# Performance work log

Measured on AMD Instinct MI355X. Metric: run time of the kernel, lower is better.

## Reference

```python
import jax, jax.numpy as jnp
import numpy as np

B, T, D, VQ, L2, HID = 8, 2048, 768, 64, 12, 1024
K = 2 ** L2          # 4096 codebook entries
N_MID = 4            # condition_layer=6 -> 1 input + 4 middle + 1 output Linear, 5 BatchNorms
EPS_N = 1e-6
EPS_BN = 1e-5


def setup_inputs() -> dict:
    key = jax.random.key(0)
    ks = jax.random.split(key, 10)
    g = lambda i, shape, sc: jax.random.normal(ks[i], shape, jnp.float32) * sc
    return {
        "h_in": jax.random.normal(ks[0], (B, D, T), jnp.float32),
        "attn_mask": jax.random.randint(ks[1], (B, T), 0, 2, jnp.int32),
        "proj_w": g(2, (VQ, D), 0.02), "proj_b": jnp.zeros((VQ,), jnp.float32),
        "inv_w": g(3, (D, VQ), 0.02), "inv_b": jnp.zeros((D,), jnp.float32),
        "mlp_w_in": g(4, (HID, L2), 0.1), "mlp_b_in": jnp.zeros((HID,), jnp.float32),
        "mlp_w_mid": g(5, (N_MID, HID, HID), 0.03), "mlp_b_mid": jnp.zeros((N_MID, HID), jnp.float32),
        "mlp_w_out": g(6, (VQ, HID), 0.03), "mlp_b_out": jnp.zeros((VQ,), jnp.float32),
        "bn_gamma": jnp.ones((N_MID + 1, HID), jnp.float32),
        "bn_beta": jnp.zeros((N_MID + 1, HID), jnp.float32),
    }


def _bn(x, gamma, beta):
    # BatchNorm1d, training mode: batch mean / biased var over codebook rows
    m = x.mean(axis=0)
    v = x.var(axis=0)
    return (x - m) * jax.lax.rsqrt(v + EPS_BN) * gamma + beta


def _l2norm(x):
    return x / (jnp.linalg.norm(x, axis=-1, keepdims=True) + EPS_N)


def reference(h_in, attn_mask, proj_w, proj_b, inv_w, inv_b,
              mlp_w_in, mlp_b_in, mlp_w_mid, mlp_b_mid, mlp_w_out, mlp_b_out,
              bn_gamma, bn_beta):
    # --- codebook: binary vectors -> condition MLP (Linear+BN+ReLU x5, Linear) ---
    ints = jnp.arange(K)
    bits = ((ints[:, None] & (1 << jnp.arange(L2 - 1, -1, -1))) > 0).astype(jnp.float32)  # [K, L2]
    x = jax.nn.relu(_bn(bits @ mlp_w_in.T + mlp_b_in, bn_gamma[0], bn_beta[0]))
    for i in range(N_MID):
        x = jax.nn.relu(_bn(x @ mlp_w_mid[i].T + mlp_b_mid[i], bn_gamma[i + 1], bn_beta[i + 1]))
    embed = x @ mlp_w_out.T + mlp_b_out          # [K, VQ]
    embed = _l2norm(embed)                        # sphere=True

    # --- project hidden states: h_in [B,D,T] -> [B,T,VQ] ---
    h = jnp.einsum('bdt,vd->btv', h_in, proj_w) + proj_b
    h = _l2norm(h)

    # --- pairwise squared distances to codebook, argmax of -d (== softmax argmax) ---
    hf = h.reshape(-1, VQ)                                       # [B*T, VQ]
    d = (hf ** 2).sum(-1, keepdims=True) + (embed ** 2).sum(-1) - 2.0 * (hf @ embed.T)  # [B*T, K]
    code = jnp.argmax(-d, axis=-1)                               # [B*T]

    # --- masked gather/scatter quantization (eval path: hard codes) ---
    mask = (attn_mask == 1)                                      # [B, T]
    h_vq = embed[code].reshape(B, T, VQ) * mask[..., None].astype(h.dtype)
    quantized = jnp.einsum('btv,dv->btd', h_vq, inv_w) + inv_b   # proj_inv -> [B, T, D]
    vq_code = jnp.where(mask, code.reshape(B, T), 0)
    return quantized, vq_code
```

## Files before the change

### kernel.cpp

```cpp
#include <hip/hip_runtime.h>
#include <stddef.h>

#define BB   8
#define TT_  2048
#define DD   768
#define VQ_  64
#define L2C  12
#define HID_ 1024
#define KK   4096
#define NMID 4
#define NT   (BB*TT_)

typedef _Float16 h8v __attribute__((ext_vector_type(8)));
typedef float    f4v __attribute__((ext_vector_type(4)));

#define GL16(g, l) __builtin_amdgcn_global_load_lds( \
    (const __attribute__((address_space(1))) void*)(g), \
    (__attribute__((address_space(3))) void*)(l), 16, 0, 0)

__global__ __launch_bounds__(256) void k_mlp_in(const float* __restrict__ w_in,
                                                const float* __restrict__ b_in,
                                                float* __restrict__ X) {
    __shared__ float ws_[256 * 12];
    __shared__ float bs_[256];
    int tid = threadIdx.x;
    int h0  = blockIdx.x * 256;
    for (int i = tid; i < 256 * 12; i += 256) ws_[i] = w_in[h0 * 12 + i];
    bs_[tid] = b_in[h0 + tid];
    __syncthreads();
    float w[12];
#pragma unroll
    for (int l = 0; l < 12; l++) w[l] = ws_[tid * 12 + l];
    float bias = bs_[tid];
    int k0 = blockIdx.y * 16;
    for (int kk = 0; kk < 16; kk++) {
        int k = k0 + kk;
        float acc = bias;
#pragma unroll
        for (int l = 0; l < 12; l++)
            if ((k >> (11 - l)) & 1) acc += w[l];
        X[(size_t)k * HID_ + h0 + tid] = acc;
    }
}

__global__ __launch_bounds__(256) void k_bn_stats1(const float* __restrict__ Y,
                                                   float* __restrict__ part) {
    int b = blockIdx.x;
    int c = blockIdx.y * 256 + threadIdx.x;
    const float* src = Y + ((size_t)b << 6) * HID_ + c;
    float s = 0.f, q = 0.f;
    for (int r = 0; r < 64; r++) {
        float v = src[(size_t)r << 10];
        s += v; q += v * v;
    }
    part[((size_t)b << 10) + c] = s;
    part[65536 + ((size_t)b << 10) + c] = q;
}

__global__ __launch_bounds__(256) void k_bn_stats2(const float* __restrict__ part,
                                                   float* __restrict__ mv) {
    int c = blockIdx.x * 256 + threadIdx.x;
    float s = 0.f, q = 0.f;
    for (int b = 0; b < 64; b++) {
        s += part[((size_t)b << 10) + c];
        q += part[65536 + ((size_t)b << 10) + c];
    }
    float m = s * (1.f / KK);
    float v = q * (1.f / KK) - m * m;
    mv[c] = m; mv[HID_ + c] = v;
}

__global__ __launch_bounds__(256) void k_bn_apply_split(const float* __restrict__ Y,
                                                        const float* __restrict__ mv,
                                                        const float* __restrict__ gamma,
                                                        const float* __restrict__ beta,
                                                        _Float16* __restrict__ Xhi,
                                                        _Float16* __restrict__ Xlo) {
    int i = blockIdx.x * 256 + threadIdx.x;
    int c = (i << 2) & (HID_ - 1);
    float4 x = ((const float4*)Y)[i];
    float4 m = *(const float4*)(mv + c);
    float4 v = *(const float4*)(mv + HID_ + c);
    float4 g = *(const float4*)(gamma + c);
    float4 b = *(const float4*)(beta + c);
    float o[4];
    o[0] = fmaxf(0.f, (x.x - m.x) * (1.f / sqrtf(v.x + 1e-5f)) * g.x + b.x);
    o[1] = fmaxf(0.f, (x.y - m.y) * (1.f / sqrtf(v.y + 1e-5f)) * g.y + b.y);
    o[2] = fmaxf(0.f, (x.z - m.z) * (1.f / sqrtf(v.z + 1e-5f)) * g.z + b.z);
    o[3] = fmaxf(0.f, (x.w - m.w) * (1.f / sqrtf(v.w + 1e-5f)) * g.w + b.w);
    union { _Float16 h[4]; uint2 u; } uh, ul;
#pragma unroll
    for (int j = 0; j < 4; j++) {
        _Float16 h = (_Float16)o[j];
        uh.h[j] = h;
        ul.h[j] = (_Float16)(o[j] - (float)h);
    }
    *(uint2*)(Xhi + ((size_t)i << 2)) = uh.u;
    *(uint2*)(Xlo + ((size_t)i << 2)) = ul.u;
}

__global__ __launch_bounds__(256) void k_gemm_mfma3(const _Float16* __restrict__ Ahi,
                                                    const _Float16* __restrict__ Alo,
                                                    const _Float16* __restrict__ Whi,
                                                    const _Float16* __restrict__ Wlo,
                                                    const float* __restrict__ bias,
                                                    float* __restrict__ C) {
    __shared__ __attribute__((aligned(128))) char lds[4 * 32768];
    const int tid = threadIdx.x;
    const int wg = blockIdx.x;
    const int m0 = (wg & 31) << 7;
    const int n0 = (wg >> 5) << 7;
    const int wave = tid >> 6, lane = tid & 63;
    const int l15 = lane & 15, quad = lane >> 4;
    const int wm = (wave >> 1) << 6;
    const int wn = (wave & 1) << 6;

    const int rowA = (wave << 5) + (lane >> 2);
    const int colb = (((lane & 3) ^ (rowA & 3)) << 4);
    const char* gA_h = (const char*)Ahi + ((size_t)(m0 + rowA) << 11) + colb;
    const char* gA_l = (const char*)Alo + ((size_t)(m0 + rowA) << 11) + colb;
    const char* gW_h = (const char*)Whi + ((size_t)(n0 + rowA) << 11) + colb;
    const char* gW_l = (const char*)Wlo + ((size_t)(n0 + rowA) << 11) + colb;
    const int dA = wave << 11;

    const int rsw = l15 & 3;
    int offA[4], offW[4];
#pragma unroll
    for (int i = 0; i < 4; i++) offA[i] = ((wm + (i << 4) + l15) << 6) + ((quad ^ rsw) << 4);
#pragma unroll
    for (int j = 0; j < 4; j++) offW[j] = ((wn + (j << 4) + l15) << 6) + ((quad ^ rsw) << 4);

    f4v acc[4][4];
#pragma unroll
    for (int i = 0; i < 4; i++)
#pragma unroll
        for (int j = 0; j < 4; j++) acc[i][j] = (f4v){0.f, 0.f, 0.f, 0.f};

#define STG(bufi, tt) do { \
        char* b_ = lds + ((bufi) << 15); int o_ = (tt) << 6; \
        GL16(gA_h + o_,         b_ + dA); \
        GL16(gA_h + 32768 + o_, b_ + dA + 1024); \
        GL16(gA_l + o_,         b_ + 8192 + dA); \
        GL16(gA_l + 32768 + o_, b_ + 8192 + dA + 1024); \
        GL16(gW_h + o_,         b_ + 16384 + dA); \
        GL16(gW_h + 32768 + o_, b_ + 16384 + dA + 1024); \
        GL16(gW_l + o_,         b_ + 24576 + dA); \
        GL16(gW_l + 32768 + o_, b_ + 24576 + dA + 1024); \
    } while (0)

    STG(0, 0); STG(1, 1); STG(2, 2);
    for (int t = 0; t < 32; ++t) {
        if (t <= 29)      asm volatile("s_waitcnt vmcnt(16)" ::: "memory");
        else if (t == 30) asm volatile("s_waitcnt vmcnt(8)"  ::: "memory");
        else              asm volatile("s_waitcnt vmcnt(0)"  ::: "memory");
        __builtin_amdgcn_s_barrier();
        asm volatile("" ::: "memory");
        if (t + 3 < 32) STG((t + 3) & 3, t + 3);
        const char* b = lds + ((size_t)(t & 3) << 15);
        h8v ah[4], al[4], bh[4], bl[4];
#pragma unroll
        for (int i = 0; i < 4; i++) {
            ah[i] = *(const h8v*)(b + offA[i]);
            al[i] = *(const h8v*)(b + 8192 + offA[i]);
        }
#pragma unroll
        for (int j = 0; j < 4; j++) {
            bh[j] = *(const h8v*)(b + 16384 + offW[j]);
            bl[j] = *(const h8v*)(b + 24576 + offW[j]);
        }
        __builtin_amdgcn_s_setprio(1);
#pragma unroll
        for (int j = 0; j < 4; j++)
#pragma unroll
            for (int i = 0; i < 4; i++)
                acc[i][j] = __builtin_amdgcn_mfma_f32_16x16x32_f16(ah[i], bh[j], acc[i][j], 0, 0, 0);
#pragma unroll
        for (int j = 0; j < 4; j++)
#pragma unroll
            for (int i = 0; i < 4; i++)
                acc[i][j] = __builtin_amdgcn_mfma_f32_16x16x32_f16(ah[i], bl[j], acc[i][j], 0, 0, 0);
#pragma unroll
        for (int j = 0; j < 4; j++)
#pragma unroll
            for (int i = 0; i < 4; i++)
                acc[i][j] = __builtin_amdgcn_mfma_f32_16x16x32_f16(al[i], bh[j], acc[i][j], 0, 0, 0);
        __builtin_amdgcn_s_setprio(0);
        asm volatile("" ::: "memory");
    }
#undef STG

#pragma unroll
    for (int j = 0; j < 4; j++) {
        int col = n0 + wn + (j << 4) + l15;
        float bv = bias[col];
#pragma unroll
        for (int i = 0; i < 4; i++) {
            int row = m0 + wm + (i << 4) + (quad << 2);
#pragma unroll
            for (int r = 0; r < 4; r++)
                C[(size_t)(row + r) * HID_ + col] = acc[i][j][r] + bv;
        }
    }
}

__global__ __launch_bounds__(256) void k_gemm_mfma2(const _Float16* __restrict__ Ahi,
                                                    const _Float16* __restrict__ Alo,
                                                    const _Float16* __restrict__ Whi,
                                                    const _Float16* __restrict__ Wlo,
                                                    const float* __restrict__ bias,
                                                    float* __restrict__ C,
                                                    int M, int N, int Kd) {
    __shared__ __attribute__((aligned(128))) char lds[2][24576];
    const int tid = threadIdx.x;
    int wg = blockIdx.x;
    const int nwg = gridDim.x;
    wg = (wg & 7) * (nwg >> 3) + (wg >> 3);
    const int nx = M >> 7;
    const int m0 = (wg % nx) << 7;
    const int n0 = (wg / nx) << 6;
    const int wave = tid >> 6, lane = tid & 63;
    const int l15 = lane & 15, quad = lane >> 4;
    const int wm = (wave >> 1) << 6;
    const int wn = (wave & 1) << 5;

    const int pA0 = ((wave << 1) | 0) * 1024 + lane * 16;
    const int pA1 = ((wave << 1) | 1) * 1024 + lane * 16;
    const int pW  = wave * 1024 + lane * 16;
    const int qA0 = pA0 ^ (((pA0 >> 7) & 3) << 4);
    const int qA1 = pA1 ^ (((pA1 >> 7) & 3) << 4);
    const int qW  = pW  ^ (((pW  >> 7) & 3) << 4);
    const size_t krow = (size_t)Kd * 2;
    const char* gAh0 = (const char*)Ahi + (size_t)(m0 + (qA0 >> 6)) * krow + (qA0 & 63);
    const char* gAh1 = (const char*)Ahi + (size_t)(m0 + (qA1 >> 6)) * krow + (qA1 & 63);
    const char* gAl0 = (const char*)Alo + (size_t)(m0 + (qA0 >> 6)) * krow + (qA0 & 63);
    const char* gAl1 = (const char*)Alo + (size_t)(m0 + (qA1 >> 6)) * krow + (qA1 & 63);
    const char* gWh  = (const char*)Whi + (size_t)(n0 + (qW >> 6)) * krow + (qW & 63);
    const char* gWl  = (const char*)Wlo + (size_t)(n0 + (qW >> 6)) * krow + (qW & 63);
    const int dA0 = (wave << 1) * 1024;
    const int dA1 = dA0 + 1024;
    const int dW  = wave * 1024;

    int offA[4], offW[2];
#pragma unroll
    for (int i = 0; i < 4; i++) {
        int r = wm + (i << 4) + l15;
        offA[i] = r * 64 + ((quad ^ ((r >> 1) & 3)) << 4);
    }
#pragma unroll
    for (int j = 0; j < 2; j++) {
        int r = wn + (j << 4) + l15;
        offW[j] = r * 64 + ((quad ^ ((r >> 1) & 3)) << 4);
    }

    f4v acc[4][2];
#pragma unroll
    for (int i = 0; i < 4; i++)
#pragma unroll
        for (int j = 0; j < 2; j++) acc[i][j] = (f4v){0.f, 0.f, 0.f, 0.f};

#define STAGE(bufi, tt) do { \
        char* b_ = lds[bufi]; size_t o_ = (size_t)(tt) << 6; \
        GL16(gAh0 + o_, b_ + dA0); \
        GL16(gAh1 + o_, b_ + dA1); \
        GL16(gAl0 + o_, b_ + 8192 + dA0); \
        GL16(gAl1 + o_, b_ + 8192 + dA1); \
        GL16(gWh  + o_, b_ + 16384 + dW); \
        GL16(gWl  + o_, b_ + 20480 + dW); \
    } while (0)

    STAGE(0, 0);
    const int nt = Kd >> 5;
    for (int t = 0; t < nt; ++t) {
        const int cur = t & 1;
        if (t + 1 < nt) {
            STAGE(cur ^ 1, t + 1);
            asm volatile("s_waitcnt vmcnt(6)" ::: "memory");
        } else {
            asm volatile("s_waitcnt vmcnt(0)" ::: "memory");
        }
        __builtin_amdgcn_s_barrier();
        asm volatile("" ::: "memory");
        const char* b = lds[cur];
        h8v ah[4], al[4], bh[2], bl[2];
#pragma unroll
        for (int i = 0; i < 4; i++) {
            ah[i] = *(const h8v*)(b + offA[i]);
            al[i] = *(const h8v*)(b + 8192 + offA[i]);
        }
#pragma unroll
        for (int j = 0; j < 2; j++) {
            bh[j] = *(const h8v*)(b + 16384 + offW[j]);
            bl[j] = *(const h8v*)(b + 20480 + offW[j]);
        }
        __builtin_amdgcn_s_setprio(1);
#pragma unroll
        for (int i = 0; i < 4; i++)
#pragma unroll
            for (int j = 0; j < 2; j++)
                acc[i][j] = __builtin_amdgcn_mfma_f32_16x16x32_f16(ah[i], bh[j], acc[i][j], 0, 0, 0);
#pragma unroll
        for (int i = 0; i < 4; i++)
#pragma unroll
            for (int j = 0; j < 2; j++)
                acc[i][j] = __builtin_amdgcn_mfma_f32_16x16x32_f16(ah[i], bl[j], acc[i][j], 0, 0, 0);
#pragma unroll
        for (int i = 0; i < 4; i++)
#pragma unroll
            for (int j = 0; j < 2; j++)
                acc[i][j] = __builtin_amdgcn_mfma_f32_16x16x32_f16(al[i], bh[j], acc[i][j], 0, 0, 0);
        __builtin_amdgcn_s_setprio(0);
        asm volatile("" ::: "memory");
        __builtin_amdgcn_s_barrier();
    }
#undef STAGE

#pragma unroll
    for (int j = 0; j < 2; j++) {
        int col = n0 + wn + (j << 4) + l15;
        float bv = bias[col];
#pragma unroll
        for (int i = 0; i < 4; i++) {
            int row = m0 + wm + (i << 4) + (quad << 2);
#pragma unroll
            for (int r = 0; r < 4; r++)
                C[(size_t)(row + r) * N + col] = acc[i][j][r] + bv;
        }
    }
}

__global__ __launch_bounds__(256) void k_l2norm(float* __restrict__ E,
                                                float* __restrict__ eqh,
                                                _Float16* __restrict__ Ehi,
                                                _Float16* __restrict__ Elo) {
    int tid = threadIdx.x;
    int row = blockIdx.x * 4 + (tid >> 6);
    int v = tid & 63;
    size_t off = ((size_t)row << 6) + v;
    float x = E[off];
    float ss = x * x;
#pragma unroll
    for (int o = 32; o; o >>= 1) ss += __shfl_xor(ss, o, 64);
    float inv = 1.f / (sqrtf(ss) + 1e-6f);
    float xn = x * inv;
    E[off] = xn;
    _Float16 hh = (_Float16)xn;
    Ehi[off] = hh;
    Elo[off] = (_Float16)(xn - (float)hh);
    if (v == 0) eqh[row] = -0.5f * (ss * inv * inv);
}

__global__ __launch_bounds__(256) void k_wsplit_all(const float* __restrict__ w_mid,
                                                    const float* __restrict__ w_out,
                                                    const float* __restrict__ proj_w,
                                                    _Float16* __restrict__ Wmh,
                                                    _Float16* __restrict__ Wml,
                                                    _Float16* __restrict__ Woh,
                                                    _Float16* __restrict__ Wol,
                                                    _Float16* __restrict__ pwhi,
                                                    _Float16* __restrict__ pwlo) {
    int i = blockIdx.x * 256 + threadIdx.x;
    const float4* src; _Float16 *dh, *dl; int off;
    if (i < 1048576)            { src = (const float4*)w_mid;  dh = Wmh;  dl = Wml;  off = i; }
    else if (i < 1048576+16384) { src = (const float4*)w_out;  dh = Woh;  dl = Wol;  off = i - 1048576; }
    else                        { src = (const float4*)proj_w; dh = pwhi; dl = pwlo; off = i - 1048576 - 16384; }
    float4 w = src[off];
    float wf[4] = {w.x, w.y, w.z, w.w};
    union { _Float16 h[4]; uint2 u; } uh, ul;
#pragma unroll
    for (int j = 0; j < 4; j++) {
        _Float16 h = (_Float16)wf[j];
        uh.h[j] = h;
        ul.h[j] = (_Float16)(wf[j] - (float)h);
    }
    *(uint2*)(dh + ((size_t)off << 2)) = uh.u;
    *(uint2*)(dl + ((size_t)off << 2)) = ul.u;
}

__global__ __launch_bounds__(256) void k_cvt_inv(const float* __restrict__ iw,
                                                 _Float16* __restrict__ iwh) {
    int i = blockIdx.x * 256 + threadIdx.x;
    float4 w = ((const float4*)iw)[i];
    union { _Float16 h[4]; uint2 u; } uh;
    uh.h[0] = (_Float16)w.x; uh.h[1] = (_Float16)w.y;
    uh.h[2] = (_Float16)w.z; uh.h[3] = (_Float16)w.w;
    *(uint2*)(iwh + ((size_t)i << 2)) = uh.u;
}

__global__ __launch_bounds__(256) void k_proj_mfma(const float* __restrict__ h_in,
                                                   const _Float16* __restrict__ pwhi,
                                                   const _Float16* __restrict__ pwlo,
                                                   float* __restrict__ Hpart) {
    __shared__ float shA[128 * 33];
    const int tid = threadIdx.x;
    const int t0 = blockIdx.x * 128;
    const int ks = blockIdx.y;
    const int b = t0 >> 11;
    const int tloc0 = t0 & (TT_ - 1);
    const int wave = tid >> 6, lane = tid & 63;
    const int l15 = lane & 15, quad = lane >> 4;

    const int dl = tid >> 3;
    const int tg = (tid & 7) << 4;

    f4v acc[2][4];
#pragma unroll
    for (int i = 0; i < 2; i++)
#pragma unroll
        for (int j = 0; j < 4; j++) acc[i][j] = (f4v){0.f, 0.f, 0.f, 0.f};

    for (int kk = 0; kk < 6; kk++) {
        int dd0 = ks * 192 + kk * 32;
        const float* src = h_in + ((size_t)(b * DD + dd0 + dl) << 11) + tloc0 + tg;
        float4 g0 = *(const float4*)(src);
        float4 g1 = *(const float4*)(src + 4);
        float4 g2 = *(const float4*)(src + 8);
        float4 g3 = *(const float4*)(src + 12);
        __syncthreads();
        float gv[16] = {g0.x, g0.y, g0.z, g0.w, g1.x, g1.y, g1.z, g1.w,
                        g2.x, g2.y, g2.z, g2.w, g3.x, g3.y, g3.z, g3.w};
#pragma unroll
        for (int i = 0; i < 16; i++) shA[(tg + i) * 33 + dl] = gv[i];
        __syncthreads();

        h8v ah[2], al[2];
#pragma unroll
        for (int mt = 0; mt < 2; mt++) {
            const float* ap = &shA[((wave << 5) + (mt << 4) + l15) * 33 + (quad << 3)];
            float4 a0 = *(const float4*)(ap);
            float4 a1 = *(const float4*)(ap + 4);
            float av[8] = {a0.x, a0.y, a0.z, a0.w, a1.x, a1.y, a1.z, a1.w};
#pragma unroll
            for (int j = 0; j < 8; j++) {
                _Float16 h = (_Float16)av[j];
                ah[mt][j] = h;
                al[mt][j] = (_Float16)(av[j] - (float)h);
            }
        }
        h8v bh[4], bl[4];
#pragma unroll
        for (int nt = 0; nt < 4; nt++) {
            size_t wb = (size_t)((nt << 4) + l15) * DD + dd0 + (quad << 3);
            bh[nt] = *(const h8v*)(pwhi + wb);
            bl[nt] = *(const h8v*)(pwlo + wb);
        }
#pragma unroll
        for (int nt = 0; nt < 4; nt++)
#pragma unroll
            for (int mt = 0; mt < 2; mt++)
                acc[mt][nt] = __builtin_amdgcn_mfma_f32_16x16x32_f16(ah[mt], bh[nt], acc[mt][nt], 0, 0, 0);
#pragma unroll
        for (int nt = 0; nt < 4; nt++)
#pragma unroll
            for (int mt = 0; mt < 2; mt++)
                acc[mt][nt] = __builtin_amdgcn_mfma_f32_16x16x32_f16(ah[mt], bl[nt], acc[mt][nt], 0, 0, 0);
#pragma unroll
        for (int nt = 0; nt < 4; nt++)
#pragma unroll
            for (int mt = 0; mt < 2; mt++)
                acc[mt][nt] = __builtin_amdgcn_mfma_f32_16x16x32_f16(al[mt], bh[nt], acc[mt][nt], 0, 0, 0);
    }
    float* dst = Hpart + ((size_t)ks << 20);
#pragma unroll
    for (int mt = 0; mt < 2; mt++) {
#pragma unroll
        for (int r = 0; r < 4; r++) {
            int t = t0 + (wave << 5) + (mt << 4) + (quad << 2) + r;
#pragma unroll
            for (int nt = 0; nt < 4; nt++)
                dst[((size_t)t << 6) + (nt << 4) + l15] = acc[mt][nt][r];
        }
    }
}

__global__ __launch_bounds__(256) void k_hnorm(const float* __restrict__ Hpart,
                                               const float* __restrict__ pb,
                                               _Float16* __restrict__ Hhi,
                                               _Float16* __restrict__ Hlo) {
    __shared__ float ssp[4][64];
    int tid = threadIdx.x;
    int tt = tid & 63, vg = tid >> 6;
    int t = blockIdx.x * 64 + tt;
    size_t base = ((size_t)t << 6) + (vg << 4);
    float o[16];
#pragma unroll
    for (int u = 0; u < 4; u++) {
        float4 p0 = *(const float4*)(Hpart + (0u << 20) + base + (u << 2));
        float4 p1 = *(const float4*)(Hpart + (1u << 20) + base + (u << 2));
        float4 p2 = *(const float4*)(Hpart + (2u << 20) + base + (u << 2));
        float4 p3 = *(const float4*)(Hpart + (3u << 20) + base + (u << 2));
        o[u * 4 + 0] = p0.x + p1.x + p2.x + p3.x;
        o[u * 4 + 1] = p0.y + p1.y + p2.y + p3.y;
        o[u * 4 + 2] = p0.z + p1.z + p2.z + p3.z;
        o[u * 4 + 3] = p0.w + p1.w + p2.w + p3.w;
    }
    float sp = 0.f;
#pragma unroll
    for (int j = 0; j < 16; j++) {
        o[j] += pb[(vg << 4) + j];
        sp = fmaf(o[j], o[j], sp);
    }
    ssp[vg][tt] = sp;
    __syncthreads();
    float ss = ssp[0][tt] + ssp[1][tt] + ssp[2][tt] + ssp[3][tt];
    float inv = 1.f / (sqrtf(ss) + 1e-6f);
    union { _Float16 h[8]; uint4 u; } uh0, uh1, ul0, ul1;
#pragma unroll
    for (int j = 0; j < 16; j++) {
        float xn = o[j] * inv;
        _Float16 hh = (_Float16)xn;
        _Float16 ll = (_Float16)(xn - (float)hh);
        if (j < 8) { uh0.h[j] = hh; ul0.h[j] = ll; }
        else       { uh1.h[j - 8] = hh; ul1.h[j - 8] = ll; }
    }
    *(uint4*)(Hhi + base)     = uh0.u;
    *(uint4*)(Hhi + base + 8) = uh1.u;
    *(uint4*)(Hlo + base)     = ul0.u;
    *(uint4*)(Hlo + base + 8) = ul1.u;
}

__global__ __launch_bounds__(256, 4) void k_argmax_mfma(const _Float16* __restrict__ Hhi,
                                                        const _Float16* __restrict__ Hlo,
                                                        const _Float16* __restrict__ Ehi,
                                                        const _Float16* __restrict__ Elo,
                                                        const float* __restrict__ eqh,
                                                        float* __restrict__ ps,
                                                        int* __restrict__ pi) {
    __shared__ __attribute__((aligned(128))) char elds[4 * 4096 + 1024];
    int tid = threadIdx.x;
    int wave = tid >> 6, lane = tid & 63;
    int l15 = lane & 15, quad = lane >> 4;
    int t0 = blockIdx.x * 256 + wave * 64;
    int kh = blockIdx.y;
    const int kbase = kh << 8;

    h8v hh0[4], hh1[4], hl0[4], hl1[4];
#pragma unroll
    for (int s = 0; s < 4; s++) {
        size_t hb = (size_t)(t0 + (s << 4) + l15) * 64 + (quad << 3);
        hh0[s] = *(const h8v*)(Hhi + hb);
        hh1[s] = *(const h8v*)(Hhi + hb + 32);
        hl0[s] = *(const h8v*)(Hlo + hb);
        hl1[s] = *(const h8v*)(Hlo + hb + 32);
    }
    float best[4] = {-1e30f, -1e30f, -1e30f, -1e30f};
    int   idx[4]  = {0, 0, 0, 0};

    const int p    = ((wave & 1) << 10) + lane * 16;
    const int srow = p >> 7;
    const int scol = (p & 127) ^ ((srow & 7) << 4);
    const char* gsrc0 = (const char*)((wave < 2) ? Ehi : Elo)
                      + (((size_t)kbase + srow) << 7) + scol;
    const int dwave = wave << 10;
#define ASTG(tt) GL16(gsrc0 + ((size_t)(tt) << 11), elds + (((tt) & 3) << 12) + dwave)

    const int rswz = (l15 & 7) << 4;
    const int o_e0 = l15 * 128 + ((quad << 4) ^ rswz);
    const int o_e1 = l15 * 128 + ((64 + (quad << 4)) ^ rswz);

    if (wave == 0) GL16((const char*)eqh + ((size_t)kbase << 2), elds + 16384);
    ASTG(0); ASTG(1); ASTG(2);

    for (int t = 0; t < 16; ++t) {
        if (t <= 13)      asm volatile("s_waitcnt vmcnt(2)" ::: "memory");
        else if (t == 14) asm volatile("s_waitcnt vmcnt(1)" ::: "memory");
        else              asm volatile("s_waitcnt vmcnt(0)" ::: "memory");
        __builtin_amdgcn_s_barrier();
        asm volatile("" ::: "memory");
        if (t + 3 < 16) ASTG(t + 3);
        const char* b = elds + ((size_t)(t & 3) << 12);
        h8v ce0 = *(const h8v*)(b + o_e0);
        h8v ce1 = *(const h8v*)(b + o_e1);
        h8v cl0 = *(const h8v*)(b + 2048 + o_e0);
        h8v cl1 = *(const h8v*)(b + 2048 + o_e1);
        float4 cq = *(const float4*)(elds + 16384 + (t << 6) + (quad << 4));
        int k0 = kbase + (t << 4);

        f4v acc[4];
#pragma unroll
        for (int s = 0; s < 4; s++) acc[s] = (f4v){0.f, 0.f, 0.f, 0.f};
        __builtin_amdgcn_s_setprio(1);
#pragma unroll
        for (int s = 0; s < 4; s++) acc[s] = __builtin_amdgcn_mfma_f32_16x16x32_f16(ce0, hh0[s], acc[s], 0, 0, 0);
#pragma unroll
        for (int s = 0; s < 4; s++) acc[s] = __builtin_amdgcn_mfma_f32_16x16x32_f16(ce1, hh1[s], acc[s], 0, 0, 0);
#pragma unroll
        for (int s = 0; s < 4; s++) acc[s] = __builtin_amdgcn_mfma_f32_16x16x32_f16(cl0, hh0[s], acc[s], 0, 0, 0);
#pragma unroll
        for (int s = 0; s < 4; s++) acc[s] = __builtin_amdgcn_mfma_f32_16x16x32_f16(cl1, hh1[s], acc[s], 0, 0, 0);
#pragma unroll
        for (int s = 0; s < 4; s++) acc[s] = __builtin_amdgcn_mfma_f32_16x16x32_f16(ce0, hl0[s], acc[s], 0, 0, 0);
#pragma unroll
        for (int s = 0; s < 4; s++) acc[s] = __builtin_amdgcn_mfma_f32_16x16x32_f16(ce1, hl1[s], acc[s], 0, 0, 0);
        __builtin_amdgcn_s_setprio(0);
        float qv[4] = {cq.x, cq.y, cq.z, cq.w};
#pragma unroll
        for (int r = 0; r < 4; r++) {
            int k = k0 + (quad << 2) + r;
#pragma unroll
            for (int s = 0; s < 4; s++) {
                float sc = acc[s][r] + qv[r];
                if (sc > best[s]) { best[s] = sc; idx[s] = k; }
            }
        }
        asm volatile("" ::: "memory");
    }
#undef ASTG

#pragma unroll
    for (int m = 16; m <= 32; m <<= 1) {
#pragma unroll
        for (int s = 0; s < 4; s++) {
            float ob = __shfl_xor(best[s], m, 64);
            int   oi = __shfl_xor(idx[s], m, 64);
            if (ob > best[s] || (ob == best[s] && oi < idx[s])) { best[s] = ob; idx[s] = oi; }
        }
    }
    if (quad == 0) {
#pragma unroll
        for (int s = 0; s < 4; s++) {
            int t = t0 + (s << 4) + l15;
            ps[(size_t)t * 16 + kh] = best[s];
            pi[(size_t)t * 16 + kh] = idx[s];
        }
    }
}

__global__ __launch_bounds__(256) void k_merge(const float* __restrict__ ps,
                                               const int* __restrict__ pi,
                                               const int* __restrict__ mask,
                                               const _Float16* __restrict__ Ehi,
                                               _Float16* __restrict__ G16,
                                               float* __restrict__ outc) {
    __shared__ int codes[256];
    __shared__ int ms[256];
    int tid = threadIdx.x;
    int base = blockIdx.x << 8;
    int t = base + tid;
    float best = ps[(size_t)t * 16];
    int bi = pi[(size_t)t * 16];
#pragma unroll
    for (int s = 1; s < 16; s++) {
        float v = ps[(size_t)t * 16 + s];
        if (v > best) { best = v; bi = pi[(size_t)t * 16 + s]; }
    }
    int m = mask[t];
    codes[tid] = bi;
    ms[tid] = m;
    outc[t] = m ? (float)bi : 0.0f;
    __syncthreads();
    for (int i = tid; i < 256 * 8; i += 256) {
        int r = i >> 3, u = i & 7;
        uint4 e = ms[r] ? ((const uint4*)(Ehi + ((size_t)codes[r] << 6)))[u]
                        : make_uint4(0u, 0u, 0u, 0u);
        ((uint4*)(G16 + ((size_t)(base + r) << 6)))[u] = e;
    }
}

__global__ __launch_bounds__(256) void k_gemm_out(const _Float16* __restrict__ G16,
                                                  const _Float16* __restrict__ iwh,
                                                  const float* __restrict__ bias,
                                                  float* __restrict__ C) {
    const int tid = threadIdx.x;
    const int t0 = blockIdx.x * 128, n0 = blockIdx.y * 64;
    const int wave = tid >> 6, lane = tid & 63;
    const int l15 = lane & 15, quad = lane >> 4;

    f4v acc[2][4];
#pragma unroll
    for (int i = 0; i < 2; i++)
#pragma unroll
        for (int j = 0; j < 4; j++) acc[i][j] = (f4v){0.f, 0.f, 0.f, 0.f};

#pragma unroll
    for (int ks = 0; ks < 2; ks++) {
        int kk = (ks << 5) + (quad << 3);
        h8v a[2], b[4];
#pragma unroll
        for (int mt = 0; mt < 2; mt++)
            a[mt] = *(const h8v*)(G16 + (size_t)(t0 + (wave << 5) + (mt << 4) + l15) * 64 + kk);
#pragma unroll
        for (int nt = 0; nt < 4; nt++)
            b[nt] = *(const h8v*)(iwh + (size_t)(n0 + (nt << 4) + l15) * 64 + kk);
#pragma unroll
        for (int mt = 0; mt < 2; mt++)
#pragma unroll
            for (int nt = 0; nt < 4; nt++)
                acc[mt][nt] = __builtin_amdgcn_mfma_f32_16x16x32_f16(a[mt], b[nt], acc[mt][nt], 0, 0, 0);
    }
#pragma unroll
    for (int nt = 0; nt < 4; nt++) {
        int col = n0 + (nt << 4) + l15;
        float bv = bias[col];
#pragma unroll
        for (int mt = 0; mt < 2; mt++) {
            int row = t0 + (wave << 5) + (mt << 4) + (quad << 2);
#pragma unroll
            for (int r = 0; r < 4; r++)
                C[(size_t)(row + r) * DD + col] = acc[mt][nt][r] + bv;
        }
    }
}

extern "C" void kernel_launch(void* const* d_in, const int* in_sizes, int n_in,
                              void* d_out, int out_size, void* d_ws, size_t ws_size,
                              hipStream_t stream) {
    const float* h_in   = (const float*)d_in[0];
    const int*   amask  = (const int*)d_in[1];
    const float* proj_w = (const float*)d_in[2];
    const float* proj_b = (const float*)d_in[3];
    const float* inv_w  = (const float*)d_in[4];
    const float* inv_b  = (const float*)d_in[5];
    const float* w_in   = (const float*)d_in[6];
    const float* b_in   = (const float*)d_in[7];
    const float* w_mid  = (const float*)d_in[8];
    const float* b_mid  = (const float*)d_in[9];
    const float* w_out  = (const float*)d_in[10];
    const float* b_out  = (const float*)d_in[11];
    const float* gamma  = (const float*)d_in[12];
    const float* beta   = (const float*)d_in[13];

    float*     Y    = (float*)d_ws;
    _Float16*  Xhi  = (_Float16*)(Y + (size_t)KK * HID_);
    _Float16*  Xlo  = Xhi + (size_t)KK * HID_;
    float*     mv   = (float*)(Xlo + (size_t)KK * HID_);
    float*     Emb  = mv + 2 * HID_;
    float*     eqh  = Emb + (size_t)KK * VQ_;
    float*     spart= eqh + KK;
    _Float16*  pwhi = (_Float16*)(spart + 2 * 65536);
    _Float16*  pwlo = pwhi + (size_t)VQ_ * DD;
    float*    Hpart = Y;
    _Float16* H16hi = Xhi;
    _Float16* H16lo = H16hi + (size_t)NT * VQ_;
    _Float16* E16hi = H16lo + (size_t)NT * VQ_;
    _Float16* E16lo = E16hi + (size_t)KK * VQ_;
    float*    ps    = (float*)(E16lo + (size_t)KK * VQ_);
    int*      pidx  = (int*)(ps + (size_t)NT * 16);
    _Float16* G16   = (_Float16*)(pidx + (size_t)NT * 16);
    _Float16* iwh   = G16 + (size_t)NT * VQ_;

    float* out_q = (float*)d_out;
    float* out_c = out_q + (size_t)NT * DD;

    _Float16* Wmh = (_Float16*)d_out;
    _Float16* Wml = Wmh + (size_t)NMID * HID_ * HID_;
    _Float16* Woh = Wml + (size_t)NMID * HID_ * HID_;
    _Float16* Wol = Woh + (size_t)VQ_ * HID_;

    k_wsplit_all<<<4208, 256, 0, stream>>>(w_mid, w_out, proj_w,
                                           Wmh, Wml, Woh, Wol, pwhi, pwlo);

    k_mlp_in<<<dim3(HID_ / 256, KK / 16), 256, 0, stream>>>(w_in, b_in, Y);
    k_bn_stats1<<<dim3(64, 4), 256, 0, stream>>>(Y, spart);
    k_bn_stats2<<<4, 256, 0, stream>>>(spart, mv);
    k_bn_apply_split<<<KK * HID_ / 1024, 256, 0, stream>>>(Y, mv, gamma, beta, Xhi, Xlo);
    for (int i = 0; i < NMID; i++) {
        k_gemm_mfma3<<<(KK / 128) * (HID_ / 128), 256, 0, stream>>>(
            Xhi, Xlo, Wmh + (size_t)i * HID_ * HID_, Wml + (size_t)i * HID_ * HID_,
            b_mid + (size_t)i * HID_, Y);
        k_bn_stats1<<<dim3(64, 4), 256, 0, stream>>>(Y, spart);
        k_bn_stats2<<<4, 256, 0, stream>>>(spart, mv);
        k_bn_apply_split<<<KK * HID_ / 1024, 256, 0, stream>>>(Y, mv,
            gamma + (size_t)(i + 1) * HID_, beta + (size_t)(i + 1) * HID_, Xhi, Xlo);
    }
    k_gemm_mfma2<<<(KK / 128) * (VQ_ / 64), 256, 0, stream>>>(
        Xhi, Xlo, Woh, Wol, b_out, Emb, KK, VQ_, HID_);
    k_l2norm<<<KK / 4, 256, 0, stream>>>(Emb, eqh, E16hi, E16lo);

    k_cvt_inv<<<VQ_ * DD / 1024, 256, 0, stream>>>(inv_w, iwh);
    k_proj_mfma<<<dim3(NT / 128, 4), 256, 0, stream>>>(h_in, pwhi, pwlo, Hpart);
    k_hnorm<<<NT / 64, 256, 0, stream>>>(Hpart, proj_b, H16hi, H16lo);
    k_argmax_mfma<<<dim3(NT / 256, 16), 256, 0, stream>>>(
        H16hi, H16lo, E16hi, E16lo, eqh, ps, pidx);
    k_merge<<<NT / 256, 256, 0, stream>>>(ps, pidx, amask, E16hi, G16, out_c);
    k_gemm_out<<<dim3(NT / 128, DD / 64), 256, 0, stream>>>(G16, iwh, inv_b, out_q);
}
```

Measured before the change: 454.2 us.

## Rebalance GEMM pipelines: double-buffer mfma3, triple-buffer mfma2 with 64-wide K tiles

The 128x128 split-fp16 GEMM drops from a 4-stage LDS ring to a 2-stage double buffer with an extra barrier, cutting its LDS footprint from 128 KB to 64 KB. The 128x64 generic GEMM goes the other way: it now stages 64-wide K tiles with an 8-way XOR swizzle into a 3-deep ring, issuing loads two tiles ahead and removing the trailing barrier. The aim is to hide load latency better in mfma2 and raise occupancy or reduce LDS pressure in mfma3. The trade-off is less prefetch depth in mfma3 and 144 KB of LDS in mfma2, which limits it to one block per CU.

```diff
diff --git a/kernel.cpp b/kernel.cpp
--- a/kernel.cpp
+++ b/kernel.cpp
@@ -105,7 +105,7 @@
                                                     const _Float16* __restrict__ Wlo,
                                                     const float* __restrict__ bias,
                                                     float* __restrict__ C) {
-    __shared__ __attribute__((aligned(128))) char lds[4 * 32768];
+    __shared__ __attribute__((aligned(128))) char lds[2 * 32768];
     const int tid = threadIdx.x;
     const int wg = blockIdx.x;
     const int m0 = (wg & 31) << 7;
@@ -148,15 +148,17 @@
         GL16(gW_l + 32768 + o_, b_ + 24576 + dA + 1024); \
     } while (0)
 
-    STG(0, 0); STG(1, 1); STG(2, 2);
+    STG(0, 0);
     for (int t = 0; t < 32; ++t) {
-        if (t <= 29)      asm volatile("s_waitcnt vmcnt(16)" ::: "memory");
-        else if (t == 30) asm volatile("s_waitcnt vmcnt(8)"  ::: "memory");
-        else              asm volatile("s_waitcnt vmcnt(0)"  ::: "memory");
+        if (t + 1 < 32) {
+            STG((t + 1) & 1, t + 1);
+            asm volatile("s_waitcnt vmcnt(8)" ::: "memory");
+        } else {
+            asm volatile("s_waitcnt vmcnt(0)" ::: "memory");
+        }
         __builtin_amdgcn_s_barrier();
         asm volatile("" ::: "memory");
-        if (t + 3 < 32) STG((t + 3) & 3, t + 3);
-        const char* b = lds + ((size_t)(t & 3) << 15);
+        const char* b = lds + ((size_t)(t & 1) << 15);
         h8v ah[4], al[4], bh[4], bl[4];
 #pragma unroll
         for (int i = 0; i < 4; i++) {
@@ -186,6 +188,7 @@
                 acc[i][j] = __builtin_amdgcn_mfma_f32_16x16x32_f16(al[i], bh[j], acc[i][j], 0, 0, 0);
         __builtin_amdgcn_s_setprio(0);
         asm volatile("" ::: "memory");
+        __builtin_amdgcn_s_barrier();
     }
 #undef STG
 
@@ -210,7 +213,7 @@
                                                     const float* __restrict__ bias,
                                                     float* __restrict__ C,
                                                     int M, int N, int Kd) {
-    __shared__ __attribute__((aligned(128))) char lds[2][24576];
+    __shared__ __attribute__((aligned(128))) char lds[3 * 49152];
     const int tid = threadIdx.x;
     int wg = blockIdx.x;
     const int nwg = gridDim.x;
@@ -223,33 +226,30 @@
     const int wm = (wave >> 1) << 6;
     const int wn = (wave & 1) << 5;
 
-    const int pA0 = ((wave << 1) | 0) * 1024 + lane * 16;
-    const int pA1 = ((wave << 1) | 1) * 1024 + lane * 16;
-    const int pW  = wave * 1024 + lane * 16;
-    const int qA0 = pA0 ^ (((pA0 >> 7) & 3) << 4);
-    const int qA1 = pA1 ^ (((pA1 >> 7) & 3) << 4);
-    const int qW  = pW  ^ (((pW  >> 7) & 3) << 4);
     const size_t krow = (size_t)Kd * 2;
-    const char* gAh0 = (const char*)Ahi + (size_t)(m0 + (qA0 >> 6)) * krow + (qA0 & 63);
-    const char* gAh1 = (const char*)Ahi + (size_t)(m0 + (qA1 >> 6)) * krow + (qA1 & 63);
-    const char* gAl0 = (const char*)Alo + (size_t)(m0 + (qA0 >> 6)) * krow + (qA0 & 63);
-    const char* gAl1 = (const char*)Alo + (size_t)(m0 + (qA1 >> 6)) * krow + (qA1 & 63);
-    const char* gWh  = (const char*)Whi + (size_t)(n0 + (qW >> 6)) * krow + (qW & 63);
-    const char* gWl  = (const char*)Wlo + (size_t)(n0 + (qW >> 6)) * krow + (qW & 63);
-    const int dA0 = (wave << 1) * 1024;
-    const int dA1 = dA0 + 1024;
-    const int dW  = wave * 1024;
-
-    int offA[4], offW[2];
+    const int colb2 = (((lane & 7) ^ (lane >> 3)) << 4);
+    const char* gA_h = (const char*)Ahi + (size_t)(m0 + (wave << 5) + (lane >> 3)) * krow + colb2;
+    const char* gA_l = (const char*)Alo + (size_t)(m0 + (wave << 5) + (lane >> 3)) * krow + colb2;
+    const char* gW_h = (const char*)Whi + (size_t)(n0 + (wave << 4) + (lane >> 3)) * krow + colb2;
+    const char* gW_l = (const char*)Wlo + (size_t)(n0 + (wave << 4) + (lane >> 3)) * krow + colb2;
+    const int dAh = wave << 12;
+    const int dWh = wave << 11;
+    const size_t g8 = 8 * krow;
+
+    int offA[4][2], offW[2][2];
 #pragma unroll
     for (int i = 0; i < 4; i++) {
         int r = wm + (i << 4) + l15;
-        offA[i] = r * 64 + ((quad ^ ((r >> 1) & 3)) << 4);
+        int sw = (r & 7) << 4;
+        offA[i][0] = (r << 7) + (((quad << 4)) ^ sw);
+        offA[i][1] = (r << 7) + ((64 | (quad << 4)) ^ sw);
     }
 #pragma unroll
     for (int j = 0; j < 2; j++) {
         int r = wn + (j << 4) + l15;
-        offW[j] = r * 64 + ((quad ^ ((r >> 1) & 3)) << 4);
+        int sw = (r & 7) << 4;
+        offW[j][0] = (r << 7) + (((quad << 4)) ^ sw);
+        offW[j][1] = (r << 7) + ((64 | (quad << 4)) ^ sw);
     }
 
     f4v acc[4][2];
@@ -258,61 +258,65 @@
 #pragma unroll
         for (int j = 0; j < 2; j++) acc[i][j] = (f4v){0.f, 0.f, 0.f, 0.f};
 
-#define STAGE(bufi, tt) do { \
-        char* b_ = lds[bufi]; size_t o_ = (size_t)(tt) << 6; \
-        GL16(gAh0 + o_, b_ + dA0); \
-        GL16(gAh1 + o_, b_ + dA1); \
-        GL16(gAl0 + o_, b_ + 8192 + dA0); \
-        GL16(gAl1 + o_, b_ + 8192 + dA1); \
-        GL16(gWh  + o_, b_ + 16384 + dW); \
-        GL16(gWl  + o_, b_ + 20480 + dW); \
+#define STG2(bufi, tt) do { \
+        char* b_ = lds + (size_t)(bufi) * 49152; size_t o_ = (size_t)(tt) << 7; \
+        GL16(gA_h + o_,            b_ + dAh); \
+        GL16(gA_h + g8 + o_,       b_ + dAh + 1024); \
+        GL16(gA_h + 2*g8 + o_,     b_ + dAh + 2048); \
+        GL16(gA_h + 3*g8 + o_,     b_ + dAh + 3072); \
+        GL16(gA_l + o_,            b_ + 16384 + dAh); \
+        GL16(gA_l + g8 + o_,       b_ + 16384 + dAh + 1024); \
+        GL16(gA_l + 2*g8 + o_,     b_ + 16384 + dAh + 2048); \
+        GL16(gA_l + 3*g8 + o_,     b_ + 16384 + dAh + 3072); \
+        GL16(gW_h + o_,            b_ + 32768 + dWh); \
+        GL16(gW_h + g8 + o_,       b_ + 32768 + dWh + 1024); \
+        GL16(gW_l + o_,            b_ + 40960 + dWh); \
+        GL16(gW_l + g8 + o_,       b_ + 40960 + dWh + 1024); \
     } while (0)
 
-    STAGE(0, 0);
-    const int nt = Kd >> 5;
+    const int nt = Kd >> 6;
+    STG2(0, 0); STG2(1, 1);
     for (int t = 0; t < nt; ++t) {
-        const int cur = t & 1;
-        if (t + 1 < nt) {
-            STAGE(cur ^ 1, t + 1);
-            asm volatile("s_waitcnt vmcnt(6)" ::: "memory");
-        } else {
-            asm volatile("s_waitcnt vmcnt(0)" ::: "memory");
-        }
+        if (t <= nt - 2) asm volatile("s_waitcnt vmcnt(12)" ::: "memory");
+        else             asm volatile("s_waitcnt vmcnt(0)"  ::: "memory");
         __builtin_amdgcn_s_barrier();
         asm volatile("" ::: "memory");
-        const char* b = lds[cur];
-        h8v ah[4], al[4], bh[2], bl[2];
-#pragma unroll
-        for (int i = 0; i < 4; i++) {
-            ah[i] = *(const h8v*)(b + offA[i]);
-            al[i] = *(const h8v*)(b + 8192 + offA[i]);
-        }
-#pragma unroll
-        for (int j = 0; j < 2; j++) {
-            bh[j] = *(const h8v*)(b + 16384 + offW[j]);
-            bl[j] = *(const h8v*)(b + 20480 + offW[j]);
-        }
-        __builtin_amdgcn_s_setprio(1);
-#pragma unroll
-        for (int i = 0; i < 4; i++)
-#pragma unroll
-            for (int j = 0; j < 2; j++)
-                acc[i][j] = __builtin_amdgcn_mfma_f32_16x16x32_f16(ah[i], bh[j], acc[i][j], 0, 0, 0);
-#pragma unroll
-        for (int i = 0; i < 4; i++)
-#pragma unroll
-            for (int j = 0; j < 2; j++)
-                acc[i][j] = __builtin_amdgcn_mfma_f32_16x16x32_f16(ah[i], bl[j], acc[i][j], 0, 0, 0);
-#pragma unroll
-        for (int i = 0; i < 4; i++)
-#pragma unroll
-            for (int j = 0; j < 2; j++)
-                acc[i][j] = __builtin_amdgcn_mfma_f32_16x16x32_f16(al[i], bh[j], acc[i][j], 0, 0, 0);
-        __builtin_amdgcn_s_setprio(0);
+        if (t + 2 < nt) STG2((t + 2) % 3, t + 2);
+        const char* b = lds + (size_t)(t % 3) * 49152;
+#pragma unroll
+        for (int s = 0; s < 2; s++) {
+            h8v ah[4], al[4], bh[2], bl[2];
+#pragma unroll
+            for (int i = 0; i < 4; i++) {
+                ah[i] = *(const h8v*)(b + offA[i][s]);
+                al[i] = *(const h8v*)(b + 16384 + offA[i][s]);
+            }
+#pragma unroll
+            for (int j = 0; j < 2; j++) {
+                bh[j] = *(const h8v*)(b + 32768 + offW[j][s]);
+                bl[j] = *(const h8v*)(b + 40960 + offW[j][s]);
+            }
+            __builtin_amdgcn_s_setprio(1);
+#pragma unroll
+            for (int i = 0; i < 4; i++)
+#pragma unroll
+                for (int j = 0; j < 2; j++)
+                    acc[i][j] = __builtin_amdgcn_mfma_f32_16x16x32_f16(ah[i], bh[j], acc[i][j], 0, 0, 0);
+#pragma unroll
+            for (int i = 0; i < 4; i++)
+#pragma unroll
+                for (int j = 0; j < 2; j++)
+                    acc[i][j] = __builtin_amdgcn_mfma_f32_16x16x32_f16(ah[i], bl[j], acc[i][j], 0, 0, 0);
+#pragma unroll
+            for (int i = 0; i < 4; i++)
+#pragma unroll
+                for (int j = 0; j < 2; j++)
+                    acc[i][j] = __builtin_amdgcn_mfma_f32_16x16x32_f16(al[i], bh[j], acc[i][j], 0, 0, 0);
+            __builtin_amdgcn_s_setprio(0);
+        }
         asm volatile("" ::: "memory");
-        __builtin_amdgcn_s_barrier();
-    }
-#undef STAGE
+    }
+#undef STG2
 
 #pragma unroll
     for (int j = 0; j < 2; j++) {
```

Measured after the change: 464.6 us. 1.02x slower.

## Fuse BN stats/apply into cooperative grid kernel and merge small launches

Applied to the files above, without the earlier changes.

Merges the weight split and input MLP layer into one launch. It also merges the embedding L2-norm with the inverse-weight conversion. The three BatchNorm kernels (partial stats, reduce, apply) become one cooperative kernel that uses grid-wide syncs. The aim is to cut kernel launch overhead and inter-kernel gaps across the five BN layers, at the cost of grid barrier latency and a fixed 256-block grid that does each apply slice serially in 16 steps.

```diff
diff --git a/kernel.cpp b/kernel.cpp
--- a/kernel.cpp
+++ b/kernel.cpp
@@ -1,5 +1,8 @@
 #include <hip/hip_runtime.h>
+#include <hip/hip_cooperative_groups.h>
 #include <stddef.h>
+
+namespace cg = cooperative_groups;
 
 #define BB   8
 #define TT_  2048
@@ -18,85 +21,119 @@
     (const __attribute__((address_space(1))) void*)(g), \
     (__attribute__((address_space(3))) void*)(l), 16, 0, 0)
 
-__global__ __launch_bounds__(256) void k_mlp_in(const float* __restrict__ w_in,
-                                                const float* __restrict__ b_in,
-                                                float* __restrict__ X) {
+__global__ __launch_bounds__(256) void k_init(const float* __restrict__ w_in,
+                                              const float* __restrict__ b_in,
+                                              float* __restrict__ X,
+                                              const float* __restrict__ w_mid,
+                                              const float* __restrict__ w_out,
+                                              const float* __restrict__ proj_w,
+                                              _Float16* __restrict__ Wmh,
+                                              _Float16* __restrict__ Wml,
+                                              _Float16* __restrict__ Woh,
+                                              _Float16* __restrict__ Wol,
+                                              _Float16* __restrict__ pwhi,
+                                              _Float16* __restrict__ pwlo) {
     __shared__ float ws_[256 * 12];
     __shared__ float bs_[256];
-    int tid = threadIdx.x;
-    int h0  = blockIdx.x * 256;
-    for (int i = tid; i < 256 * 12; i += 256) ws_[i] = w_in[h0 * 12 + i];
-    bs_[tid] = b_in[h0 + tid];
-    __syncthreads();
-    float w[12];
-#pragma unroll
-    for (int l = 0; l < 12; l++) w[l] = ws_[tid * 12 + l];
-    float bias = bs_[tid];
-    int k0 = blockIdx.y * 16;
-    for (int kk = 0; kk < 16; kk++) {
-        int k = k0 + kk;
-        float acc = bias;
-#pragma unroll
-        for (int l = 0; l < 12; l++)
-            if ((k >> (11 - l)) & 1) acc += w[l];
-        X[(size_t)k * HID_ + h0 + tid] = acc;
-    }
-}
-
-__global__ __launch_bounds__(256) void k_bn_stats1(const float* __restrict__ Y,
-                                                   float* __restrict__ part) {
-    int b = blockIdx.x;
-    int c = blockIdx.y * 256 + threadIdx.x;
-    const float* src = Y + ((size_t)b << 6) * HID_ + c;
-    float s = 0.f, q = 0.f;
-    for (int r = 0; r < 64; r++) {
-        float v = src[(size_t)r << 10];
-        s += v; q += v * v;
-    }
-    part[((size_t)b << 10) + c] = s;
-    part[65536 + ((size_t)b << 10) + c] = q;
-}
-
-__global__ __launch_bounds__(256) void k_bn_stats2(const float* __restrict__ part,
-                                                   float* __restrict__ mv) {
-    int c = blockIdx.x * 256 + threadIdx.x;
-    float s = 0.f, q = 0.f;
-    for (int b = 0; b < 64; b++) {
-        s += part[((size_t)b << 10) + c];
-        q += part[65536 + ((size_t)b << 10) + c];
-    }
-    float m = s * (1.f / KK);
-    float v = q * (1.f / KK) - m * m;
-    mv[c] = m; mv[HID_ + c] = v;
-}
-
-__global__ __launch_bounds__(256) void k_bn_apply_split(const float* __restrict__ Y,
-                                                        const float* __restrict__ mv,
-                                                        const float* __restrict__ gamma,
-                                                        const float* __restrict__ beta,
-                                                        _Float16* __restrict__ Xhi,
-                                                        _Float16* __restrict__ Xlo) {
-    int i = blockIdx.x * 256 + threadIdx.x;
-    int c = (i << 2) & (HID_ - 1);
-    float4 x = ((const float4*)Y)[i];
-    float4 m = *(const float4*)(mv + c);
-    float4 v = *(const float4*)(mv + HID_ + c);
-    float4 g = *(const float4*)(gamma + c);
-    float4 b = *(const float4*)(beta + c);
-    float o[4];
-    o[0] = fmaxf(0.f, (x.x - m.x) * (1.f / sqrtf(v.x + 1e-5f)) * g.x + b.x);
-    o[1] = fmaxf(0.f, (x.y - m.y) * (1.f / sqrtf(v.y + 1e-5f)) * g.y + b.y);
-    o[2] = fmaxf(0.f, (x.z - m.z) * (1.f / sqrtf(v.z + 1e-5f)) * g.z + b.z);
-    o[3] = fmaxf(0.f, (x.w - m.w) * (1.f / sqrtf(v.w + 1e-5f)) * g.w + b.w);
-    union { _Float16 h[4]; uint2 u; } uh, ul;
-#pragma unroll
-    for (int j = 0; j < 4; j++) {
-        _Float16 h = (_Float16)o[j];
-        uh.h[j] = h;
-        ul.h[j] = (_Float16)(o[j] - (float)h);
-    }
-    *(uint2*)(Xhi + ((size_t)i << 2)) = uh.u;
-    *(uint2*)(Xlo + ((size_t)i << 2)) = ul.u;
+    const int bid = blockIdx.x;
+    const int tid = threadIdx.x;
+    if (bid < 4208) {
+        int i = bid * 256 + tid;
+        const float4* src; _Float16 *dh, *dl; int off;
+        if (i < 1048576)            { src = (const float4*)w_mid;  dh = Wmh;  dl = Wml;  off = i; }
+        else if (i < 1048576+16384) { src = (const float4*)w_out;  dh = Woh;  dl = Wol;  off = i - 1048576; }
+        else                        { src = (const float4*)proj_w; dh = pwhi; dl = pwlo; off = i - 1048576 - 16384; }
+        float4 w = src[off];
+        float wf[4] = {w.x, w.y, w.z, w.w};
+        union { _Float16 h[4]; uint2 u; } uh, ul;
+#pragma unroll
+        for (int j = 0; j < 4; j++) {
+            _Float16 h = (_Float16)wf[j];
+            uh.h[j] = h;
+            ul.h[j] = (_Float16)(wf[j] - (float)h);
+        }
+        *(uint2*)(dh + ((size_t)off << 2)) = uh.u;
+        *(uint2*)(dl + ((size_t)off << 2)) = ul.u;
+    } else {
+        int b2 = bid - 4208;
+        int h0 = (b2 & 3) << 8;
+        int k0 = (b2 >> 2) << 4;
+        for (int i = tid; i < 256 * 12; i += 256) ws_[i] = w_in[h0 * 12 + i];
+        bs_[tid] = b_in[h0 + tid];
+        __syncthreads();
+        float w[12];
+#pragma unroll
+        for (int l = 0; l < 12; l++) w[l] = ws_[tid * 12 + l];
+        float bias = bs_[tid];
+        for (int kk = 0; kk < 16; kk++) {
+            int k = k0 + kk;
+            float acc = bias;
+#pragma unroll
+            for (int l = 0; l < 12; l++)
+                if ((k >> (11 - l)) & 1) acc += w[l];
+            X[(size_t)k * HID_ + h0 + tid] = acc;
+        }
+    }
+}
+
+__global__ __launch_bounds__(256) void k_bn_stack(const float* __restrict__ Y,
+                                                  float* __restrict__ part,
+                                                  float* __restrict__ mv,
+                                                  const float* __restrict__ gamma,
+                                                  const float* __restrict__ beta,
+                                                  _Float16* __restrict__ Xhi,
+                                                  _Float16* __restrict__ Xlo) {
+    cg::grid_group gg = cg::this_grid();
+    const int tid = threadIdx.x;
+    const int bid = blockIdx.x;
+    {
+        int b = bid >> 2;
+        int c = ((bid & 3) << 8) + tid;
+        const float* src = Y + ((size_t)b << 6) * HID_ + c;
+        float s = 0.f, q = 0.f;
+        for (int r = 0; r < 64; r++) {
+            float v = src[(size_t)r << 10];
+            s += v; q += v * v;
+        }
+        part[((size_t)b << 10) + c] = s;
+        part[65536 + ((size_t)b << 10) + c] = q;
+    }
+    gg.sync();
+    if (bid < 4) {
+        int c = (bid << 8) + tid;
+        float s = 0.f, q = 0.f;
+        for (int b = 0; b < 64; b++) {
+            s += part[((size_t)b << 10) + c];
+            q += part[65536 + ((size_t)b << 10) + c];
+        }
+        float m = s * (1.f / KK);
+        float v = q * (1.f / KK) - m * m;
+        mv[c] = m; mv[HID_ + c] = v;
+    }
+    gg.sync();
+    for (int sl = 0; sl < 16; sl++) {
+        int i = (((bid << 4) + sl) << 8) + tid;
+        int c = (i << 2) & (HID_ - 1);
+        float4 x = ((const float4*)Y)[i];
+        float4 m = *(const float4*)(mv + c);
+        float4 v = *(const float4*)(mv + HID_ + c);
+        float4 g = *(const float4*)(gamma + c);
+        float4 b = *(const float4*)(beta + c);
+        float o[4];
+        o[0] = fmaxf(0.f, (x.x - m.x) * (1.f / sqrtf(v.x + 1e-5f)) * g.x + b.x);
+        o[1] = fmaxf(0.f, (x.y - m.y) * (1.f / sqrtf(v.y + 1e-5f)) * g.y + b.y);
+        o[2] = fmaxf(0.f, (x.z - m.z) * (1.f / sqrtf(v.z + 1e-5f)) * g.z + b.z);
+        o[3] = fmaxf(0.f, (x.w - m.w) * (1.f / sqrtf(v.w + 1e-5f)) * g.w + b.w);
+        union { _Float16 h[4]; uint2 u; } uh, ul;
+#pragma unroll
+        for (int j = 0; j < 4; j++) {
+            _Float16 h = (_Float16)o[j];
+            uh.h[j] = h;
+            ul.h[j] = (_Float16)(o[j] - (float)h);
+        }
+        *(uint2*)(Xhi + ((size_t)i << 2)) = uh.u;
+        *(uint2*)(Xlo + ((size_t)i << 2)) = ul.u;
+    }
 }
 
 __global__ __launch_bounds__(256) void k_gemm_mfma3(const _Float16* __restrict__ Ahi,
@@ -328,62 +365,37 @@
     }
 }
 
-__global__ __launch_bounds__(256) void k_l2norm(float* __restrict__ E,
-                                                float* __restrict__ eqh,
-                                                _Float16* __restrict__ Ehi,
-                                                _Float16* __restrict__ Elo) {
+__global__ __launch_bounds__(256) void k_l2norm_cvt(float* __restrict__ E,
+                                                    float* __restrict__ eqh,
+                                                    _Float16* __restrict__ Ehi,
+                                                    _Float16* __restrict__ Elo,
+                                                    const float* __restrict__ iw,
+                                                    _Float16* __restrict__ iwh) {
+    int bid = blockIdx.x;
     int tid = threadIdx.x;
-    int row = blockIdx.x * 4 + (tid >> 6);
-    int v = tid & 63;
-    size_t off = ((size_t)row << 6) + v;
-    float x = E[off];
-    float ss = x * x;
-#pragma unroll
-    for (int o = 32; o; o >>= 1) ss += __shfl_xor(ss, o, 64);
-    float inv = 1.f / (sqrtf(ss) + 1e-6f);
-    float xn = x * inv;
-    E[off] = xn;
-    _Float16 hh = (_Float16)xn;
-    Ehi[off] = hh;
-    Elo[off] = (_Float16)(xn - (float)hh);
-    if (v == 0) eqh[row] = -0.5f * (ss * inv * inv);
-}
-
-__global__ __launch_bounds__(256) void k_wsplit_all(const float* __restrict__ w_mid,
-                                                    const float* __restrict__ w_out,
-                                                    const float* __restrict__ proj_w,
-                                                    _Float16* __restrict__ Wmh,
-                                                    _Float16* __restrict__ Wml,
-                                                    _Float16* __restrict__ Woh,
-                                                    _Float16* __restrict__ Wol,
-                                                    _Float16* __restrict__ pwhi,
-                                                    _Float16* __restrict__ pwlo) {
-    int i = blockIdx.x * 256 + threadIdx.x;
-    const float4* src; _Float16 *dh, *dl; int off;
-    if (i < 1048576)            { src = (const float4*)w_mid;  dh = Wmh;  dl = Wml;  off = i; }
-    else if (i < 1048576+16384) { src = (const float4*)w_out;  dh = Woh;  dl = Wol;  off = i - 1048576; }
-    else                        { src = (const float4*)proj_w; dh = pwhi; dl = pwlo; off = i - 1048576 - 16384; }
-    float4 w = src[off];
-    float wf[4] = {w.x, w.y, w.z, w.w};
-    union { _Float16 h[4]; uint2 u; } uh, ul;
-#pragma unroll
-    for (int j = 0; j < 4; j++) {
-        _Float16 h = (_Float16)wf[j];
-        uh.h[j] = h;
-        ul.h[j] = (_Float16)(wf[j] - (float)h);
-    }
-    *(uint2*)(dh + ((size_t)off << 2)) = uh.u;
-    *(uint2*)(dl + ((size_t)off << 2)) = ul.u;
-}
-
-__global__ __launch_bounds__(256) void k_cvt_inv(const float* __restrict__ iw,
-                                                 _Float16* __restrict__ iwh) {
-    int i = blockIdx.x * 256 + threadIdx.x;
-    float4 w = ((const float4*)iw)[i];
-    union { _Float16 h[4]; uint2 u; } uh;
-    uh.h[0] = (_Float16)w.x; uh.h[1] = (_Float16)w.y;
-    uh.h[2] = (_Float16)w.z; uh.h[3] = (_Float16)w.w;
-    *(uint2*)(iwh + ((size_t)i << 2)) = uh.u;
+    if (bid < KK / 4) {
+        int row = bid * 4 + (tid >> 6);
+        int v = tid & 63;
+        size_t off = ((size_t)row << 6) + v;
+        float x = E[off];
+        float ss = x * x;
+#pragma unroll
+        for (int o = 32; o; o >>= 1) ss += __shfl_xor(ss, o, 64);
+        float inv = 1.f / (sqrtf(ss) + 1e-6f);
+        float xn = x * inv;
+        E[off] = xn;
+        _Float16 hh = (_Float16)xn;
+        Ehi[off] = hh;
+        Elo[off] = (_Float16)(xn - (float)hh);
+        if (v == 0) eqh[row] = -0.5f * (ss * inv * inv);
+    } else {
+        int i = (bid - KK / 4) * 256 + tid;
+        float4 w = ((const float4*)iw)[i];
+        union { _Float16 h[4]; uint2 u; } uh;
+        uh.h[0] = (_Float16)w.x; uh.h[1] = (_Float16)w.y;
+        uh.h[2] = (_Float16)w.z; uh.h[3] = (_Float16)w.w;
+        *(uint2*)(iwh + ((size_t)i << 2)) = uh.u;
+    }
 }
 
 __global__ __launch_bounds__(256) void k_proj_mfma(const float* __restrict__ h_in,
@@ -746,27 +758,32 @@
     _Float16* Woh = Wml + (size_t)NMID * HID_ * HID_;
     _Float16* Wol = Woh + (size_t)VQ_ * HID_;
 
-    k_wsplit_all<<<4208, 256, 0, stream>>>(w_mid, w_out, proj_w,
-                                           Wmh, Wml, Woh, Wol, pwhi, pwlo);
-
-    k_mlp_in<<<dim3(HID_ / 256, KK / 16), 256, 0, stream>>>(w_in, b_in, Y);
-    k_bn_stats1<<<dim3(64, 4), 256, 0, stream>>>(Y, spart);
-    k_bn_stats2<<<4, 256, 0, stream>>>(spart, mv);
-    k_bn_apply_split<<<KK * HID_ / 1024, 256, 0, stream>>>(Y, mv, gamma, beta, Xhi, Xlo);
+    k_init<<<5232, 256, 0, stream>>>(w_in, b_in, Y, w_mid, w_out, proj_w,
+                                     Wmh, Wml, Woh, Wol, pwhi, pwlo);
+
+    {
+        const float* gp = gamma; const float* bp = beta;
+        void* aa[] = {(void*)&Y, (void*)&spart, (void*)&mv, (void*)&gp,
+                      (void*)&bp, (void*)&Xhi, (void*)&Xlo};
+        hipLaunchCooperativeKernel((void*)k_bn_stack, dim3(256), dim3(256),
+                                   aa, 0, stream);
+    }
     for (int i = 0; i < NMID; i++) {
         k_gemm_mfma3<<<(KK / 128) * (HID_ / 128), 256, 0, stream>>>(
             Xhi, Xlo, Wmh + (size_t)i * HID_ * HID_, Wml + (size_t)i * HID_ * HID_,
             b_mid + (size_t)i * HID_, Y);
-        k_bn_stats1<<<dim3(64, 4), 256, 0, stream>>>(Y, spart);
-        k_bn_stats2<<<4, 256, 0, stream>>>(spart, mv);
-        k_bn_apply_split<<<KK * HID_ / 1024, 256, 0, stream>>>(Y, mv,
-            gamma + (size_t)(i + 1) * HID_, beta + (size_t)(i + 1) * HID_, Xhi, Xlo);
+        const float* gp = gamma + (size_t)(i + 1) * HID_;
+        const float* bp = beta + (size_t)(i + 1) * HID_;
+        void* aa[] = {(void*)&Y, (void*)&spart, (void*)&mv, (void*)&gp,
+                      (void*)&bp, (void*)&Xhi, (void*)&Xlo};
+        hipLaunchCooperativeKernel((void*)k_bn_stack, dim3(256), dim3(256),
+                                   aa, 0, stream);
     }
     k_gemm_mfma2<<<(KK / 128) * (VQ_ / 64), 256, 0, stream>>>(
         Xhi, Xlo, Woh, Wol, b_out, Emb, KK, VQ_, HID_);
-    k_l2norm<<<KK / 4, 256, 0, stream>>>(Emb, eqh, E16hi, E16lo);
-
-    k_cvt_inv<<<VQ_ * DD / 1024, 256, 0, stream>>>(inv_w, iwh);
+    k_l2norm_cvt<<<KK / 4 + VQ_ * DD / 1024, 256, 0, stream>>>(
+        Emb, eqh, E16hi, E16lo, inv_w, iwh);
+
     k_proj_mfma<<<dim3(NT / 128, 4), 256, 0, stream>>>(h_in, pwhi, pwlo, Hpart);
     k_hnorm<<<NT / 64, 256, 0, stream>>>(Hpart, proj_b, H16hi, H16lo);
     k_argmax_mfma<<<dim3(NT / 256, 16), 256, 0, stream>>>(
```

New measurement: 785.9 us. 1.73x slower.
